# Kernel optimization log

Hardware: AMD Instinct MI355X
Metric: run time of the kernel (lower is better)

Reference implementation:

```python
import jax, jax.numpy as jnp
import numpy as np

THRESHOLD = 0.1


def _conv3x3(x, w, b):
    # x: [B,Ci,H,W], w: [Co,Ci,3,3] -> [B,Co,H,W], SAME padding, ReLU
    y = jax.lax.conv_general_dilated(
        x, w, window_strides=(1, 1), padding='SAME',
        dimension_numbers=('NCHW', 'OIHW', 'NCHW'))
    return jax.nn.relu(y + b[None, :, None, None])


def _autoencoder(x, w1, b1, w2, b2, w3, b3, w4, b4):
    h = _conv3x3(x, w1, b1)          # 64 -> 32
    mid = _conv3x3(h, w2, b2)        # 32 -> 16 (bottleneck)
    h2 = _conv3x3(mid, w3, b3)       # 16 -> 32
    rec = _conv3x3(h2, w4, b4)       # 32 -> 64
    return mid, rec


def setup_inputs() -> dict:
    key = jax.random.key(0)
    ks = jax.random.split(key, 8)
    B, C, H, W = 8, 64, 128, 256
    s = 0.05  # keep activations / singular values at a sane scale
    return {
        'feat0': jax.random.normal(ks[0], (B, C, H, W), jnp.float32),
        'feat1': jax.random.normal(ks[1], (B, C, H, W), jnp.float32),
        'w1': jax.random.normal(ks[2], (32, 64, 3, 3), jnp.float32) * s,
        'b1': jnp.zeros((32,), jnp.float32),
        'w2': jax.random.normal(ks[3], (16, 32, 3, 3), jnp.float32) * s,
        'b2': jnp.zeros((16,), jnp.float32),
        'w3': jax.random.normal(ks[4], (32, 16, 3, 3), jnp.float32) * s,
        'b3': jnp.zeros((32,), jnp.float32),
        'w4': jax.random.normal(ks[5], (64, 32, 3, 3), jnp.float32) * s,
        'b4': jnp.zeros((64,), jnp.float32),
        'modality_adapter': 0,  # accepted but unused by the original forward
    }


def reference(feat0, feat1, w1, b1, w2, b2, w3, b3, w4, b4, modality_adapter):
    feats = [feat0, feat1]
    B, C, H, W = feat0.shape
    auto_enc_loss = jnp.float32(0.0)
    counts_list = []
    for f in feats:
        mid, rec = _autoencoder(f, w1, b1, w2, b2, w3, b3, w4, b4)
        # batched SVD over [B, 16, H*W]; counts of singular values > threshold
        sv = jnp.linalg.svd(jax.lax.stop_gradient(mid.reshape(B, mid.shape[1], H * W)),
                            compute_uv=False)  # [B, 16]
        counts_list.append(jnp.sum(sv > THRESHOLD, axis=1))
        auto_enc_loss = auto_enc_loss + jnp.mean((f - rec) ** 2)
    # pick the dominant modality per batch element
    domain_idx = jnp.argmax(jnp.stack(counts_list, axis=1), axis=1)  # [B]
    con_feat = jnp.stack(feats, axis=1)                              # [B,M,C,H,W]
    dom = con_feat[jnp.arange(B), domain_idx]                        # [B,C,H,W]
    domain_features = jnp.broadcast_to(dom[:, None], con_feat.shape)  # repeat over M
    # two-stage cross-modal einsum attention
    weights = jnp.einsum('smchw,snchw->smnhw', domain_features, con_feat)
    weights = jax.nn.softmax(weights, axis=2)
    weights = jnp.einsum('smnhw,snchw->smchw', weights, con_feat)
    weights = jax.nn.softmax(weights, axis=1)
    fused_feat = jnp.sum(con_feat * weights, axis=1)  # [B,C,H,W]
    return fused_feat, auto_enc_loss
```

## Files before the change

### kernel.cpp

```cpp
#include <hip/hip_runtime.h>
#include <hip/hip_bf16.h>

#define B_ 8
#define H_ 128
#define W_ 256
#define PH 130
#define PW 258
#define NPIX (B_*64*H_*W_)

typedef short short8  __attribute__((ext_vector_type(8)));
typedef short short4v __attribute__((ext_vector_type(4)));
typedef float floatx4 __attribute__((ext_vector_type(4)));

template<int Ci, int Co, bool LOSS, bool NCHW_IN>
struct conv_cfg {
    static constexpr int SCI  = NCHW_IN ? 32 : Ci;
    static constexpr int PXB  = SCI*2;
    static constexpr int ROWW = NCHW_IN ? 68 : 66;
    static constexpr int SLAB = 6*ROWW*PXB;
    static constexpr int EPIW = 64*(Co+8)*2;
    static constexpr int RECB = 64*272*2;
    static constexpr int LDSZ = LOSS ? (RECB > SLAB ? RECB : SLAB)
                                     : (4*EPIW > SLAB ? 4*EPIW : SLAB);
};

__device__ __forceinline__
void gload_lds16(const __hip_bfloat16* g, char* l)
{
    __builtin_amdgcn_global_load_lds(
        (const __attribute__((address_space(1))) void*)g,
        (__attribute__((address_space(3))) void*)l, 16, 0, 0);
}

template<int Ci, int Co, bool LOSS, bool NCHW_IN, bool AVG>
__device__ __forceinline__
void conv_tile(int tx, int ty, int bz, int mz,
               char* __restrict__ slab, float* __restrict__ wred,
               const void* __restrict__ inA,
               const void* __restrict__ inB,
               const __hip_bfloat16* __restrict__ wt,
               const float* __restrict__ bias,
               __hip_bfloat16* __restrict__ outp,
               size_t out_mstride,
               const float* __restrict__ ref0,
               const float* __restrict__ ref1,
               const float* __restrict__ other,
               float* __restrict__ avg_out,
               float* __restrict__ acc_out)
{
    constexpr int CC   = (Ci >= 32) ? Ci/32 : 1;
    constexpr int PXB  = conv_cfg<Ci,Co,LOSS,NCHW_IN>::PXB;
    constexpr int NCB  = PXB/16;
    constexpr int ROWW = conv_cfg<Ci,Co,LOSS,NCHW_IN>::ROWW;
    constexpr int SLAB = conv_cfg<Ci,Co,LOSS,NCHW_IN>::SLAB;
    constexpr int NT   = Co/16;
    constexpr int GNT  = (NT >= 2) ? 2 : 1;
    constexpr int NG   = NT / GNT;
    constexpr int EPIW = conv_cfg<Ci,Co,LOSS,NCHW_IN>::EPIW;

    const int tid  = threadIdx.x;
    const int lane = tid & 63;
    const int wid  = tid >> 6;
    const int col  = lane & 15;
    const int quad = lane >> 4;
    const int w0   = tx * 64;
    const int h0   = ty * 4;
    const int r    = wid;

    __syncthreads();

    floatx4 acc[4][NT];
#pragma unroll
    for (int mt = 0; mt < 4; ++mt)
#pragma unroll
        for (int nt = 0; nt < NT; ++nt)
            acc[mt][nt] = (floatx4)0.f;

    auto mfma_c2 = [&](int c2) {
#pragma unroll
        for (int g = 0; g < NG; ++g) {
            short8 bfr[9*GNT];
#pragma unroll
            for (int t = 0; t < 9; ++t)
#pragma unroll
                for (int j = 0; j < GNT; ++j)
                    bfr[t*GNT+j] = *(const short8*)(wt
                        + ((size_t)(c2*9+t)*Co + (g*GNT+j)*16 + col)*32 + quad*8);
#pragma unroll
            for (int t = 0; t < 9; ++t) {
                const int dy = t/3, dx = t - (t/3)*3;
                short8 a[4];
#pragma unroll
                for (int mt = 0; mt < 4; ++mt) {
                    if constexpr (NCHW_IN) {
                        int px = (r+dy)*ROWW + mt*16 + col + dx + 1;
                        int c  = quad ^ (px & 3) ^ ((px >> 2) & 3);
                        a[mt] = *(const short8*)(slab + px*PXB + (c << 4));
                    } else {
                        int px = (r+dy)*ROWW + mt*16 + col + dx;
                        int c  = (c2*4 + quad) ^ (px & (NCB-1));
                        a[mt] = *(const short8*)(slab + px*PXB + (c << 4));
                    }
                }
#pragma unroll
                for (int j = 0; j < GNT; ++j)
#pragma unroll
                    for (int mt = 0; mt < 4; ++mt)
                        acc[mt][g*GNT+j] = __builtin_amdgcn_mfma_f32_16x16x32_bf16(
                            a[mt], bfr[t*GNT+j], acc[mt][g*GNT+j], 0, 0, 0);
            }
        }
    };

    if constexpr (NCHW_IN) {
        static_assert(Ci == 64, "NCHW staging is Ci=64 only");
        const float* src = (const float*)(mz ? inB : inA) + (size_t)bz * 64 * H_ * W_;
#pragma unroll
        for (int c2 = 0; c2 < CC; ++c2) {
            if (c2) __syncthreads();
            const float* chb = src + (size_t)(c2*32 + wid*8) * (H_*W_);
#pragma unroll
            for (int it = 0; it < 4; ++it) {
                int uu   = it*64 + lane;
                bool live = (it < 3) || (lane < 12);
                int row  = uu / 34;
                int s    = uu - row*34;
                int gh   = h0 + row - 1;
                int gw0  = w0 - 2 + 2*s;
                bool ok  = live && ((unsigned)gh < (unsigned)H_)
                                && ((unsigned)gw0 < (unsigned)(W_-1));
                const float* rp = chb + (size_t)(ok ? gh : 0)*W_ + (ok ? gw0 : 0);
                short8 v0, v1;
#pragma unroll
                for (int j = 0; j < 8; ++j) {
                    float2 f = *(const float2*)(rp + (size_t)j*(H_*W_));
                    v0[j] = __builtin_bit_cast(short,
                                __float2bfloat16(ok ? f.x : 0.f));
                    v1[j] = __builtin_bit_cast(short,
                                __float2bfloat16(ok ? f.y : 0.f));
                }
                if (live) {
                    int pxl = row*ROWW + 2*s;
                    int c0  = wid ^ (pxl & 3) ^ ((pxl >> 2) & 3);
                    *(short8*)(slab + pxl*PXB + (c0 << 4)) = v0;
                    int pxl1 = pxl + 1;
                    int c1  = wid ^ (pxl1 & 3) ^ ((pxl1 >> 2) & 3);
                    *(short8*)(slab + pxl1*PXB + (c1 << 4)) = v1;
                }
            }
            __syncthreads();
            mfma_c2(c2);
        }
    } else {
        const __hip_bfloat16* inb = (const __hip_bfloat16*)(mz ? inB : inA)
                                    + (size_t)bz * PH * PW * Ci;
        constexpr int NIT = (SLAB + 4095) / 4096;
#pragma unroll
        for (int it = 0; it < NIT; ++it) {
            int o = it*4096 + tid*16;
            if (o < SLAB) {
                int pxl = o / PXB;
                int row = pxl / ROWW;
                int pxc = pxl - row*ROWW;
                int q   = (o >> 4) & (NCB-1);
                int cb  = q ^ (pxl & (NCB-1));
                gload_lds16(inb + ((size_t)(h0+row)*PW + (w0+pxc))*Ci + cb*8,
                            slab + o);
            }
        }
        __syncthreads();

        if constexpr (Ci >= 32) {
#pragma unroll
            for (int c2 = 0; c2 < CC; ++c2)
                mfma_c2(c2);
        } else {
            short8 bfr[6*NT];
#pragma unroll
            for (int kc = 0; kc < 6; ++kc)
#pragma unroll
                for (int j = 0; j < NT; ++j)
                    bfr[kc*NT+j] = *(const short8*)(wt
                        + ((size_t)kc*Co + j*16 + col)*32 + quad*8);
#pragma unroll
            for (int kc = 0; kc < 6; ++kc) {
                const int dy = kc >> 1, half = kc & 1;
                const int dxe = half ? 2 : (quad >> 1);
                short8 a[4];
#pragma unroll
                for (int mt = 0; mt < 4; ++mt) {
                    int px = (r+dy)*ROWW + mt*16 + col + dxe;
                    a[mt] = *(const short8*)(slab + px*PXB
                              + (((quad & 1) ^ (px & 1)) << 4));
                }
#pragma unroll
                for (int j = 0; j < NT; ++j)
#pragma unroll
                    for (int mt = 0; mt < 4; ++mt)
                        acc[mt][j] = __builtin_amdgcn_mfma_f32_16x16x32_bf16(
                            a[mt], bfr[kc*NT+j], acc[mt][j], 0, 0, 0);
            }
        }
    }

    if constexpr (!LOSS) {
        __syncthreads();
        char* rt = slab + wid * EPIW;
#pragma unroll
        for (int nt = 0; nt < NT; ++nt) {
            float bv = bias[nt*16 + col];
#pragma unroll
            for (int mt = 0; mt < 4; ++mt) {
#pragma unroll
                for (int rr = 0; rr < 4; ++rr) {
                    float v = acc[mt][nt][rr] + bv;
                    v = v > 0.f ? v : 0.f;
                    int px = mt*16 + quad*4 + rr;
                    *(__hip_bfloat16*)(rt + (px*(Co+8) + nt*16 + col)*2) =
                        __float2bfloat16(v);
                }
            }
        }
        __hip_bfloat16* ob = outp + (size_t)mz * out_mstride;
        char* grow = (char*)ob
            + (((size_t)bz*PH + (h0 + r + 1))*PW + (w0 + 1))*Co*2;
        constexpr int GB = 64*Co*2;
#pragma unroll
        for (int id = 0; id < GB/1024; ++id) {
            int o  = id*1024 + lane*16;
            int px = o / (Co*2);
            int cb = o - px*(Co*2);
            *(short8*)(grow + o) = *(const short8*)(rt + px*(Co+8)*2 + cb);
        }
    } else {
        __syncthreads();
        __hip_bfloat16* rec = (__hip_bfloat16*)slab;
#pragma unroll
        for (int nt = 0; nt < NT; ++nt) {
            int co = nt*16 + col;
            float bv = bias[co];
#pragma unroll
            for (int mt = 0; mt < 4; ++mt) {
                short4v pk;
#pragma unroll
                for (int rr = 0; rr < 4; ++rr) {
                    float v = acc[mt][nt][rr] + bv;
                    v = v > 0.f ? v : 0.f;
                    pk[rr] = __builtin_bit_cast(short, __float2bfloat16(v));
                }
                *(short4v*)(rec + co*272 + r*68 + mt*16 + quad*4) = pk;
            }
        }
        __syncthreads();

        float lsum = 0.f;
        const float* refb = (mz ? ref1 : ref0) + (size_t)bz * 64 * H_ * W_;
#pragma unroll
        for (int i = 0; i < 16; ++i) {
            int row = i & 3, cg = i >> 2;
            int co  = cg*16 + wid*4 + quad;
            size_t off = ((size_t)co*H_ + h0 + row)*W_ + w0 + col*4;
            float4 f = *(const float4*)(refb + off);
            short4v pk = *(const short4v*)(rec + co*272 + row*68 + col*4);
            float d0 = f.x - __bfloat162float(__builtin_bit_cast(__hip_bfloat16, pk[0]));
            float d1 = f.y - __bfloat162float(__builtin_bit_cast(__hip_bfloat16, pk[1]));
            float d2 = f.z - __bfloat162float(__builtin_bit_cast(__hip_bfloat16, pk[2]));
            float d3 = f.w - __bfloat162float(__builtin_bit_cast(__hip_bfloat16, pk[3]));
            lsum += d0*d0 + d1*d1 + d2*d2 + d3*d3;
            if constexpr (AVG) {
                if (mz) {
                    const float* othb = other + (size_t)bz * 64 * H_ * W_;
                    float*       avgb = avg_out + (size_t)bz * 64 * H_ * W_;
                    float4 g = *(const float4*)(othb + off);
                    float4 o;
                    o.x = 0.5f*(g.x + f.x);
                    o.y = 0.5f*(g.y + f.y);
                    o.z = 0.5f*(g.z + f.z);
                    o.w = 0.5f*(g.w + f.w);
                    *(float4*)(avgb + off) = o;
                }
            }
        }
#pragma unroll
        for (int off = 32; off > 0; off >>= 1)
            lsum += __shfl_down(lsum, off, 64);
        if (lane == 0) wred[wid] = lsum;
        __syncthreads();
        if (tid == 0)
            atomicAdd(acc_out, (wred[0] + wred[1] + wred[2] + wred[3])
                               * (1.0f / (float)NPIX));
    }
}

__device__ __forceinline__
void xcd_decode(int& tx, int& ty, int& bz, int& mz)
{
    int f = (blockIdx.z*32 + blockIdx.y)*4 + blockIdx.x;
    int l = (f & 7)*256 + (f >> 3);
    tx = l & 3; ty = (l >> 2) & 31;
    int zz = l >> 7;
    bz = zz & 7; mz = zz >> 3;
}

template<int C>
__device__ __forceinline__ void zb_item(__hip_bfloat16* buf, int idx)
{
    constexpr int CP = C/8;
    int cb   = idx % CP;
    int cell = (idx / CP) % 772;
    int img  = idx / (CP*772);
    int row, colp;
    if (cell < 258)      { row = 0;   colp = cell; }
    else if (cell < 516) { row = 129; colp = cell - 258; }
    else { int r2 = cell - 516; row = 1 + (r2 >> 1); colp = (r2 & 1) ? 257 : 0; }
    short8 z = (short8)0;
    *(short8*)(buf + (((size_t)img*PH + row)*PW + colp)*C + cb*8) = z;
}

__global__ __launch_bounds__(256)
void conv1_kernel(const float* __restrict__ feat0, const float* __restrict__ feat1,
                  const __hip_bfloat16* __restrict__ WT1, const float* __restrict__ b1,
                  __hip_bfloat16* __restrict__ BUF1, __hip_bfloat16* __restrict__ BUF2,
                  size_t b1e)
{
    constexpr int LDSZ = conv_cfg<64,32,false,true>::LDSZ;
    __shared__ alignas(16) char slab[LDSZ + 32];
    __shared__ float wred[4];

    int gtid = ((blockIdx.z*gridDim.y + blockIdx.y)*gridDim.x + blockIdx.x)*256
               + threadIdx.x;
    if      (gtid < 49408) zb_item<32>(BUF1, gtid);
    else if (gtid < 74112) zb_item<16>(BUF2, gtid - 49408);

    int tx, ty, bz, mz;
    xcd_decode(tx, ty, bz, mz);
    conv_tile<64,32,false,true,false>(tx, ty, bz, mz, slab, wred,
        feat0, feat1, WT1, b1, BUF1, b1e,
        nullptr, nullptr, nullptr, nullptr, nullptr);
}

template<int Ci, int Co>
__global__ __launch_bounds__(256)
void conv_mid(const __hip_bfloat16* __restrict__ inA,
              const __hip_bfloat16* __restrict__ inB,
              const __hip_bfloat16* __restrict__ wt, const float* __restrict__ bias,
              __hip_bfloat16* __restrict__ outp, size_t out_mstride)
{
    constexpr int LDSZ = conv_cfg<Ci,Co,false,false>::LDSZ;
    __shared__ alignas(16) char slab[LDSZ + 32];
    __shared__ float wred[4];
    int tx, ty, bz, mz;
    xcd_decode(tx, ty, bz, mz);
    conv_tile<Ci,Co,false,false,false>(tx, ty, bz, mz, slab, wred,
        inA, inB, wt, bias, outp, out_mstride,
        nullptr, nullptr, nullptr, nullptr, nullptr);
}

template<bool AVG>
__global__ __launch_bounds__(256)
void conv4_kernel(const __hip_bfloat16* __restrict__ BUF1, size_t b1e,
                  const __hip_bfloat16* __restrict__ WT4, const float* __restrict__ b4,
                  const float* __restrict__ feat0, const float* __restrict__ feat1,
                  float* __restrict__ avg_out, float* __restrict__ acc)
{
    constexpr int LDSZ = conv_cfg<32,64,true,false>::LDSZ;
    __shared__ alignas(16) char slab[LDSZ + 32];
    __shared__ float wred[4];
    int tx, ty, bz, mz;
    xcd_decode(tx, ty, bz, mz);
    conv_tile<32,64,true,false,AVG>(tx, ty, bz, mz, slab, wred,
        BUF1, BUF1 + b1e, WT4, b4, nullptr, 0,
        feat0, feat1, feat0, avg_out, acc);
}

template<int Ci, int Co>
__device__ __forceinline__ void wt_item(const float* __restrict__ w,
                                        __hip_bfloat16* __restrict__ wt, int idx)
{
    int kl = idx & 31;
    int co = (idx >> 5) % Co;
    int kc = idx / (32*Co);
    float val = 0.f;
    if constexpr (Ci >= 32) {
        int c2 = kc / 9, t = kc % 9;
        int dy = t/3, dx = t%3;
        int ci = c2*32 + kl;
        val = w[((size_t)(co*Ci + ci)*3 + dy)*3 + dx];
    } else {
        int dy = kc >> 1, half = kc & 1;
        int dx = half*2 + (kl >> 4);
        int ci = kl & 15;
        if (dx < 3) val = w[((size_t)(co*Ci + ci)*3 + dy)*3 + dx];
    }
    wt[idx] = __float2bfloat16(val);
}

__global__ __launch_bounds__(256)
void setup_kernel(const float* __restrict__ w1, const float* __restrict__ w2,
                  const float* __restrict__ w3, const float* __restrict__ w4,
                  __hip_bfloat16* WT1, __hip_bfloat16* WT2,
                  __hip_bfloat16* WT3, __hip_bfloat16* WT4,
                  float* acc)
{
    int idx = blockIdx.x*256 + threadIdx.x;
    if (idx == 0) *acc = 0.f;
    if      (idx < 18432) wt_item<64,32>(w1, WT1, idx);
    else if (idx < 23040) wt_item<32,16>(w2, WT2, idx - 18432);
    else if (idx < 29184) wt_item<16,32>(w3, WT3, idx - 23040);
    else if (idx < 47616) wt_item<32,64>(w4, WT4, idx - 29184);
}

__global__ __launch_bounds__(256)
void fused_avg_kernel(const float4* __restrict__ a, const float4* __restrict__ b,
                      float4* __restrict__ o, int n4)
{
    int i = blockIdx.x*256 + threadIdx.x;
    if (i < n4) {
        float4 x = a[i], y = b[i];
        float4 r;
        r.x = 0.5f*(x.x + y.x);
        r.y = 0.5f*(x.y + y.y);
        r.z = 0.5f*(x.z + y.z);
        r.w = 0.5f*(x.w + y.w);
        o[i] = r;
    }
}

extern "C" void kernel_launch(void* const* d_in, const int* in_sizes, int n_in,
                              void* d_out, int out_size, void* d_ws, size_t ws_size,
                              hipStream_t stream)
{
    const float* feat0 = (const float*)d_in[0];
    const float* feat1 = (const float*)d_in[1];
    const float* w1 = (const float*)d_in[2];
    const float* b1 = (const float*)d_in[3];
    const float* w2 = (const float*)d_in[4];
    const float* b2 = (const float*)d_in[5];
    const float* w3 = (const float*)d_in[6];
    const float* b3 = (const float*)d_in[7];
    const float* w4 = (const float*)d_in[8];
    const float* b4 = (const float*)d_in[9];

    float* out = (float*)d_out;
    float* acc = out + NPIX;

    constexpr size_t B1B = (size_t)B_*PH*PW*32*2;
    constexpr size_t SCR_SZ = 51612672;
    const bool use_ws = (d_ws != nullptr) && (ws_size >= SCR_SZ);
    char* sb = use_ws ? (char*)d_ws : (char*)d_out;

    __hip_bfloat16* BUF1 = (__hip_bfloat16*)(sb + 0);
    __hip_bfloat16* BUF2 = (__hip_bfloat16*)(sb + 2*B1B);
    __hip_bfloat16* WT1  = (__hip_bfloat16*)(sb + 51517440);
    __hip_bfloat16* WT2  = (__hip_bfloat16*)(sb + 51554304);
    __hip_bfloat16* WT3  = (__hip_bfloat16*)(sb + 51563520);
    __hip_bfloat16* WT4  = (__hip_bfloat16*)(sb + 51575808);

    setup_kernel<<<186, 256, 0, stream>>>(w1, w2, w3, w4,
                                          WT1, WT2, WT3, WT4, acc);

    constexpr size_t B1E = B1B/2;
    constexpr size_t B2E = (size_t)B_*PH*PW*16;

    dim3 cgrid(W_/64, H_/4, 2*B_);
    dim3 blk(256);

    conv1_kernel<<<cgrid, blk, 0, stream>>>(feat0, feat1, WT1, b1,
                                            BUF1, BUF2, B1E);
    conv_mid<32,16><<<cgrid, blk, 0, stream>>>(BUF1, BUF1 + B1E, WT2, b2,
                                               BUF2, B2E);
    conv_mid<16,32><<<cgrid, blk, 0, stream>>>(BUF2, BUF2 + B2E, WT3, b3,
                                               BUF1, B1E);
    if (use_ws) {
        conv4_kernel<true><<<cgrid, blk, 0, stream>>>(BUF1, B1E, WT4, b4,
                                                      feat0, feat1, out, acc);
    } else {
        conv4_kernel<false><<<cgrid, blk, 0, stream>>>(BUF1, B1E, WT4, b4,
                                                       feat0, feat1, nullptr, acc);
        int n4 = NPIX/4;
        fused_avg_kernel<<<(n4 + 255)/256, 256, 0, stream>>>(
            (const float4*)feat0, (const float4*)feat1, (float4*)out, n4);
    }
}
```

Baseline: 318.3 us.

## Give conv1 its own kernel with 8-row tiles and two rows per wave

Conv1 gets a dedicated kernel that reads the NCHW fp32 inputs directly. Each block now covers an 8x64 output tile, with each wave computing two output rows (8 M-tiles), instead of going through the shared 4-row conv_tile path. This halves the grid and cuts the halo overhead per output row: each staged slab now has 10 rows for 8 outputs instead of 6 for 4. The weight fragments also get reused across twice as many MFMAs. In exchange, each wave holds more accumulator registers, there are fewer blocks to occupy the GPU, and the zero-border work now spreads over half as many threads.

```diff
diff --git a/kernel.cpp b/kernel.cpp
--- a/kernel.cpp
+++ b/kernel.cpp
@@ -92,15 +92,9 @@
                 short8 a[4];
 #pragma unroll
                 for (int mt = 0; mt < 4; ++mt) {
-                    if constexpr (NCHW_IN) {
-                        int px = (r+dy)*ROWW + mt*16 + col + dx + 1;
-                        int c  = quad ^ (px & 3) ^ ((px >> 2) & 3);
-                        a[mt] = *(const short8*)(slab + px*PXB + (c << 4));
-                    } else {
-                        int px = (r+dy)*ROWW + mt*16 + col + dx;
-                        int c  = (c2*4 + quad) ^ (px & (NCB-1));
-                        a[mt] = *(const short8*)(slab + px*PXB + (c << 4));
-                    }
+                    int px = (r+dy)*ROWW + mt*16 + col + dx;
+                    int c  = (c2*4 + quad) ^ (px & (NCB-1));
+                    a[mt] = *(const short8*)(slab + px*PXB + (c << 4));
                 }
 #pragma unroll
                 for (int j = 0; j < GNT; ++j)
@@ -112,46 +106,7 @@
         }
     };
 
-    if constexpr (NCHW_IN) {
-        static_assert(Ci == 64, "NCHW staging is Ci=64 only");
-        const float* src = (const float*)(mz ? inB : inA) + (size_t)bz * 64 * H_ * W_;
-#pragma unroll
-        for (int c2 = 0; c2 < CC; ++c2) {
-            if (c2) __syncthreads();
-            const float* chb = src + (size_t)(c2*32 + wid*8) * (H_*W_);
-#pragma unroll
-            for (int it = 0; it < 4; ++it) {
-                int uu   = it*64 + lane;
-                bool live = (it < 3) || (lane < 12);
-                int row  = uu / 34;
-                int s    = uu - row*34;
-                int gh   = h0 + row - 1;
-                int gw0  = w0 - 2 + 2*s;
-                bool ok  = live && ((unsigned)gh < (unsigned)H_)
-                                && ((unsigned)gw0 < (unsigned)(W_-1));
-                const float* rp = chb + (size_t)(ok ? gh : 0)*W_ + (ok ? gw0 : 0);
-                short8 v0, v1;
-#pragma unroll
-                for (int j = 0; j < 8; ++j) {
-                    float2 f = *(const float2*)(rp + (size_t)j*(H_*W_));
-                    v0[j] = __builtin_bit_cast(short,
-                                __float2bfloat16(ok ? f.x : 0.f));
-                    v1[j] = __builtin_bit_cast(short,
-                                __float2bfloat16(ok ? f.y : 0.f));
-                }
-                if (live) {
-                    int pxl = row*ROWW + 2*s;
-                    int c0  = wid ^ (pxl & 3) ^ ((pxl >> 2) & 3);
-                    *(short8*)(slab + pxl*PXB + (c0 << 4)) = v0;
-                    int pxl1 = pxl + 1;
-                    int c1  = wid ^ (pxl1 & 3) ^ ((pxl1 >> 2) & 3);
-                    *(short8*)(slab + pxl1*PXB + (c1 << 4)) = v1;
-                }
-            }
-            __syncthreads();
-            mfma_c2(c2);
-        }
-    } else {
+    {
         const __hip_bfloat16* inb = (const __hip_bfloat16*)(mz ? inB : inA)
                                     + (size_t)bz * PH * PW * Ci;
         constexpr int NIT = (SLAB + 4095) / 4096;
@@ -292,16 +247,6 @@
     }
 }
 
-__device__ __forceinline__
-void xcd_decode(int& tx, int& ty, int& bz, int& mz)
-{
-    int f = (blockIdx.z*32 + blockIdx.y)*4 + blockIdx.x;
-    int l = (f & 7)*256 + (f >> 3);
-    tx = l & 3; ty = (l >> 2) & 31;
-    int zz = l >> 7;
-    bz = zz & 7; mz = zz >> 3;
-}
-
 template<int C>
 __device__ __forceinline__ void zb_item(__hip_bfloat16* buf, int idx)
 {
@@ -323,20 +268,140 @@
                   __hip_bfloat16* __restrict__ BUF1, __hip_bfloat16* __restrict__ BUF2,
                   size_t b1e)
 {
-    constexpr int LDSZ = conv_cfg<64,32,false,true>::LDSZ;
-    __shared__ alignas(16) char slab[LDSZ + 32];
-    __shared__ float wred[4];
+    __shared__ alignas(16) char slab[43520 + 32];
+
+    const int tid  = threadIdx.x;
+    const int lane = tid & 63;
+    const int wid  = tid >> 6;
+    const int col  = lane & 15;
+    const int quad = lane >> 4;
 
     int gtid = ((blockIdx.z*gridDim.y + blockIdx.y)*gridDim.x + blockIdx.x)*256
-               + threadIdx.x;
+               + tid;
     if      (gtid < 49408) zb_item<32>(BUF1, gtid);
     else if (gtid < 74112) zb_item<16>(BUF2, gtid - 49408);
 
-    int tx, ty, bz, mz;
-    xcd_decode(tx, ty, bz, mz);
-    conv_tile<64,32,false,true,false>(tx, ty, bz, mz, slab, wred,
-        feat0, feat1, WT1, b1, BUF1, b1e,
-        nullptr, nullptr, nullptr, nullptr, nullptr);
+    int f = (blockIdx.z*gridDim.y + blockIdx.y)*gridDim.x + blockIdx.x;
+    int l = (f & 7)*128 + (f >> 3);
+    const int tx = l & 3, ty = (l >> 2) & 15;
+    const int zz = l >> 6;
+    const int bz = zz & 7, mz = zz >> 3;
+    const int w0 = tx*64, h0 = ty*8;
+
+    floatx4 acc[8][2];
+#pragma unroll
+    for (int mt = 0; mt < 8; ++mt)
+#pragma unroll
+        for (int nt = 0; nt < 2; ++nt)
+            acc[mt][nt] = (floatx4)0.f;
+
+    const float* src = (mz ? feat1 : feat0) + (size_t)bz * 64 * H_ * W_;
+
+#pragma unroll
+    for (int c2 = 0; c2 < 2; ++c2) {
+        if (c2) __syncthreads();
+        const float* chb = src + (size_t)(c2*32 + wid*8) * (H_*W_);
+#pragma unroll
+        for (int it = 0; it < 6; ++it) {
+            int uu   = it*64 + lane;
+            bool live = (it < 5) || (lane < 20);
+            int row  = uu / 34;
+            int s    = uu - row*34;
+            int gh   = h0 + row - 1;
+            int gw0  = w0 - 2 + 2*s;
+            bool ok  = live && ((unsigned)gh < (unsigned)H_)
+                            && ((unsigned)gw0 < (unsigned)(W_-1));
+            const float* rp = chb + (size_t)(ok ? gh : 0)*W_ + (ok ? gw0 : 0);
+            short8 v0, v1;
+#pragma unroll
+            for (int j = 0; j < 8; ++j) {
+                float2 fv = *(const float2*)(rp + (size_t)j*(H_*W_));
+                v0[j] = __builtin_bit_cast(short,
+                            __float2bfloat16(ok ? fv.x : 0.f));
+                v1[j] = __builtin_bit_cast(short,
+                            __float2bfloat16(ok ? fv.y : 0.f));
+            }
+            if (live) {
+                int pxl = row*68 + 2*s;
+                int c0  = wid ^ (pxl & 3) ^ ((pxl >> 2) & 3);
+                *(short8*)(slab + pxl*64 + (c0 << 4)) = v0;
+                int p1  = pxl + 1;
+                int c1  = wid ^ (p1 & 3) ^ ((p1 >> 2) & 3);
+                *(short8*)(slab + p1*64 + (c1 << 4)) = v1;
+            }
+        }
+        __syncthreads();
+
+#pragma unroll
+        for (int g = 0; g < 2; ++g) {
+            short8 bfr[9];
+#pragma unroll
+            for (int t = 0; t < 9; ++t)
+                bfr[t] = *(const short8*)(WT1
+                    + ((size_t)(c2*9+t)*32 + g*16 + col)*32 + quad*8);
+#pragma unroll
+            for (int t = 0; t < 9; ++t) {
+                const int dy = t/3, dx = t - (t/3)*3;
+#pragma unroll
+                for (int mh = 0; mh < 2; ++mh) {
+                    short8 a[4];
+#pragma unroll
+                    for (int mq = 0; mq < 4; ++mq) {
+                        int mt = mh*4 + mq;
+                        int r2 = 2*wid + (mt >> 2);
+                        int px = (r2 + dy)*68 + (mt & 3)*16 + col + dx + 1;
+                        int c  = quad ^ (px & 3) ^ ((px >> 2) & 3);
+                        a[mq] = *(const short8*)(slab + px*64 + (c << 4));
+                    }
+#pragma unroll
+                    for (int mq = 0; mq < 4; ++mq)
+                        acc[mh*4+mq][g] = __builtin_amdgcn_mfma_f32_16x16x32_bf16(
+                            a[mq], bfr[t], acc[mh*4+mq][g], 0, 0, 0);
+                }
+            }
+        }
+    }
+
+    __syncthreads();
+    char* rt = slab + wid * 10240;
+#pragma unroll
+    for (int nt = 0; nt < 2; ++nt) {
+        float bv = b1[nt*16 + col];
+#pragma unroll
+        for (int mt = 0; mt < 8; ++mt) {
+#pragma unroll
+            for (int rr = 0; rr < 4; ++rr) {
+                float v = acc[mt][nt][rr] + bv;
+                v = v > 0.f ? v : 0.f;
+                int px = (mt >> 2)*64 + (mt & 3)*16 + quad*4 + rr;
+                *(__hip_bfloat16*)(rt + (px*40 + nt*16 + col)*2) =
+                    __float2bfloat16(v);
+            }
+        }
+    }
+    __hip_bfloat16* ob = BUF1 + (size_t)mz * b1e;
+#pragma unroll
+    for (int row2 = 0; row2 < 2; ++row2) {
+        char* grow = (char*)(ob
+            + (((size_t)bz*PH + (h0 + 2*wid + row2 + 1))*PW + (w0 + 1))*32);
+#pragma unroll
+        for (int id = 0; id < 4; ++id) {
+            int o  = id*1024 + lane*16;
+            int px = o >> 6;
+            int cb = o & 63;
+            *(short8*)(grow + o) = *(const short8*)(rt + (row2*64 + px)*80 + cb);
+        }
+    }
+}
+
+__device__ __forceinline__
+void xcd_decode(int& tx, int& ty, int& bz, int& mz)
+{
+    int f = (blockIdx.z*32 + blockIdx.y)*4 + blockIdx.x;
+    int l = (f & 7)*256 + (f >> 3);
+    tx = l & 3; ty = (l >> 2) & 31;
+    int zz = l >> 7;
+    bz = zz & 7; mz = zz >> 3;
 }
 
 template<int Ci, int Co>
@@ -462,11 +527,12 @@
     constexpr size_t B1E = B1B/2;
     constexpr size_t B2E = (size_t)B_*PH*PW*16;
 
+    dim3 cgrid1(W_/64, H_/8, 2*B_);
     dim3 cgrid(W_/64, H_/4, 2*B_);
     dim3 blk(256);
 
-    conv1_kernel<<<cgrid, blk, 0, stream>>>(feat0, feat1, WT1, b1,
-                                            BUF1, BUF2, B1E);
+    conv1_kernel<<<cgrid1, blk, 0, stream>>>(feat0, feat1, WT1, b1,
+                                             BUF1, BUF2, B1E);
     conv_mid<32,16><<<cgrid, blk, 0, stream>>>(BUF1, BUF1 + B1E, WT2, b2,
                                                BUF2, B2E);
     conv_mid<16,32><<<cgrid, blk, 0, stream>>>(BUF2, BUF2 + B2E, WT3, b3,
```

Measured after the change: 314.1 us. About the same (-1.3%).
